# Kernel tuning notes

Measured on AMD Instinct MI355X. Metric: run time of the kernel, lower is better.

The kernel has to match this reference:

```python
import jax, jax.numpy as jnp
from jax import lax
import numpy as np

H = 32  # hidden size
IN = 3  # input dim
NCLASS = 7
T = 30  # sequence length used by forward (indexes t=29)


def _lstm_layer(x, W_ih, W_hh, b_ih, b_hh):
    """One unidirectional LSTM layer, batch_first x: [B,T,D] -> [B,T,H].
    PyTorch gate order: i, f, g, o."""
    B = x.shape[0]
    # Precompute input contribution for all timesteps: [B,T,4H]
    xg = jnp.einsum('btd,gd->btg', x, W_ih) + b_ih + b_hh

    def step(carry, xg_t):
        h, c = carry
        gates = xg_t + h @ W_hh.T  # [B,4H]
        i, f, g, o = jnp.split(gates, 4, axis=-1)
        i = jax.nn.sigmoid(i)
        f = jax.nn.sigmoid(f)
        g = jnp.tanh(g)
        o = jax.nn.sigmoid(o)
        c = f * c + i * g
        h = o * jnp.tanh(c)
        return (h, c), h

    h0 = jnp.zeros((B, H), x.dtype)
    (_, _), hs = lax.scan(step, (h0, h0), jnp.swapaxes(xg, 0, 1))  # hs: [T,B,H]
    return jnp.swapaxes(hs, 0, 1)


def setup_inputs() -> dict:
    key = jax.random.key(0)
    ks = jax.random.split(key, 20)
    B = 65536
    s = 1.0 / np.sqrt(H)  # PyTorch LSTM/Linear init scale
    u = lambda k, shape: jax.random.uniform(k, shape, jnp.float32, -s, s)
    inp = {'X': jax.random.normal(ks[0], (B, T, IN), jnp.float32)}
    dims_in = [IN, H, H]
    for l in range(3):
        inp[f'W_ih{l}'] = u(ks[1 + 4 * l], (4 * H, dims_in[l]))
        inp[f'W_hh{l}'] = u(ks[2 + 4 * l], (4 * H, H))
        inp[f'b_ih{l}'] = u(ks[3 + 4 * l], (4 * H,))
        inp[f'b_hh{l}'] = u(ks[4 + 4 * l], (4 * H,))
    inp['W1'] = u(ks[13], (H // 2, H))
    inp['b1'] = u(ks[14], (H // 2,))
    inp['W2'] = u(ks[15], (NCLASS, H // 2))
    inp['b2'] = u(ks[16], (NCLASS,))
    return inp


def reference(X, W_ih0, W_hh0, b_ih0, b_hh0, W_ih1, W_hh1, b_ih1, b_hh1,
              W_ih2, W_hh2, b_ih2, b_hh2, W1, b1, W2, b2):
    h = _lstm_layer(X, W_ih0, W_hh0, b_ih0, b_hh0)
    h = _lstm_layer(h, W_ih1, W_hh1, b_ih1, b_hh1)
    h = _lstm_layer(h, W_ih2, W_hh2, b_ih2, b_hh2)
    last = h[:, T - 1, :]  # [B,H]
    out = last @ W1.T + b1
    out = out @ W2.T + b2  # [B,7]; Softmax is defined but not applied in forward
    return out
```

## Files before the change

kernel.cpp:

```cpp
#include <hip/hip_runtime.h>
#include <stdint.h>

#define T_STEPS 30
#define BTOT 65536
#define L2E 1.4426950408889634f

typedef __bf16 bf16_t;
typedef bf16_t bf16x8 __attribute__((ext_vector_type(8)));
typedef float f32x4 __attribute__((ext_vector_type(4)));

__device__ __forceinline__ float exp2_fast(float x) {
#if __has_builtin(__builtin_amdgcn_exp2f)
    return __builtin_amdgcn_exp2f(x);
#else
    return __expf(x * 0.6931471805599453f);
#endif
}
__device__ __forceinline__ float rcp_fast(float x) {
    return __builtin_amdgcn_rcpf(x);
}

template <int LI, bool SAVE>
__device__ __forceinline__ void cell(
    int lane, int lrow, int kgrp,
    const bf16_t* __restrict__ wb,
    const float (&bs)[3][8],
    bf16x8 ain,
    bf16x8& ah,
    float (&cst)[3][2][4],
    float (&hsave)[2][4],
    bf16_t* __restrict__ hb)
{
    constexpr int WIH_OFF = ((LI == 0) ? 0 : (LI == 1) ? 2 : 4) * 4096;
    constexpr int WHH_OFF = WIH_OFF + 4096;

    f32x4 z;
    z[0] = 0.0f; z[1] = 0.0f; z[2] = 0.0f; z[3] = 0.0f;
    f32x4 acc[8];
#pragma unroll
    for (int tl = 0; tl < 8; ++tl) {
        bf16x8 bfr = *(const bf16x8*)(wb + WIH_OFF + (tl << 9) + (lane << 3));
        acc[tl] = __builtin_amdgcn_mfma_f32_16x16x32_bf16(ain, bfr, z, 0, 0, 0);
    }
#pragma unroll
    for (int tl = 0; tl < 8; ++tl) {
        bf16x8 bfr = *(const bf16x8*)(wb + WHH_OFF + (tl << 9) + (lane << 3));
        acc[tl] = __builtin_amdgcn_mfma_f32_16x16x32_bf16(ah, bfr, acc[tl], 0, 0, 0);
    }
#pragma unroll
    for (int mt = 0; mt < 2; ++mt) {
#pragma unroll
        for (int r = 0; r < 4; ++r) {
            const float Ae = exp2_fast(acc[0 + mt][r] * (-L2E) + bs[LI][0 + mt]);
            const float Fe = exp2_fast(acc[2 + mt][r] * (-L2E) + bs[LI][2 + mt]);
            const float Be = exp2_fast(acc[4 + mt][r] * (-2.0f * L2E) + bs[LI][4 + mt]);
            const float Oe = exp2_fast(acc[6 + mt][r] * (-L2E) + bs[LI][6 + mt]);
            const float pA = 1.0f + Ae, pF = 1.0f + Fe, pB = 1.0f + Be, pO = 1.0f + Oe;
            const float nB = 1.0f - Be;
            const float t1 = pA * pB;
            const float D  = t1 * pF;
            const float N  = __builtin_fmaf(cst[LI][mt][r], t1, nB * pF);
            const float cc = N * rcp_fast(D);
            cst[LI][mt][r] = cc;
            const float Ce = exp2_fast(cc * (-2.0f * L2E));
            const float pC = 1.0f + Ce, nC = 1.0f - Ce;
            const float hv = nC * rcp_fast(pO * pC);
            if (SAVE) hsave[mt][r] = hv;
            hb[(kgrp * 4 + r) * 40 + mt * 16 + lrow] = (bf16_t)hv;
        }
    }
    ah = *(const bf16x8*)(hb + lrow * 40 + (kgrp << 3));
}

__global__ __launch_bounds__(512, 4) void lstm3_fused(
    const float* __restrict__ X,
    const float* __restrict__ Wih0, const float* __restrict__ Whh0,
    const float* __restrict__ bih0, const float* __restrict__ bhh0,
    const float* __restrict__ Wih1, const float* __restrict__ Whh1,
    const float* __restrict__ bih1, const float* __restrict__ bhh1,
    const float* __restrict__ Wih2, const float* __restrict__ Whh2,
    const float* __restrict__ bih2, const float* __restrict__ bhh2,
    const float* __restrict__ W1, const float* __restrict__ b1,
    const float* __restrict__ W2, const float* __restrict__ b2,
    float* __restrict__ out)
{
    __shared__ alignas(16) bf16_t wfrag[6 * 4096];
    __shared__ float bias_s[3][128];
    __shared__ alignas(16) bf16_t hbuf[8][16 * 40];
    __shared__ float hfin[8][16][33];

    const int tid = threadIdx.x;

    auto stage = [&](int mat, const float* __restrict__ w, int K) {
        for (int p = tid; p < 4096; p += 512) {
            const int tile = p >> 9;
            const int r = p & 511;
            const int ln = r >> 3;
            const int j = r & 7;
            const int k = ((ln >> 4) << 3) + j;
            const int n = (tile << 4) + (ln & 15);
            const float v = (k < K) ? w[n * K + k] : 0.0f;
            wfrag[mat * 4096 + p] = (bf16_t)v;
        }
    };
    stage(0, Wih0, 3);
    stage(1, Whh0, 32);
    stage(2, Wih1, 32);
    stage(3, Whh1, 32);
    stage(4, Wih2, 32);
    stage(5, Whh2, 32);
    for (int p = tid; p < 384; p += 512) {
        const int l = p >> 7, n = p & 127;
        float v;
        if (l == 0)      v = bih0[n] + bhh0[n];
        else if (l == 1) v = bih1[n] + bhh1[n];
        else             v = bih2[n] + bhh2[n];
        bias_s[l][n] = v;
    }
    __syncthreads();

    const int wave = tid >> 6;
    const int lane = tid & 63;
    const int lrow = lane & 15;
    const int kgrp = lane >> 4;
    const int b0   = blockIdx.x * 128 + wave * 16;

    float bs[3][8];
#pragma unroll
    for (int l = 0; l < 3; ++l)
#pragma unroll
        for (int tl = 0; tl < 8; ++tl)
            bs[l][tl] = bias_s[l][tl * 16 + lrow] *
                        (((tl >> 1) == 2) ? (-2.0f * L2E) : (-L2E));

    float cst[3][2][4];
    float h2keep[2][4];
#pragma unroll
    for (int l = 0; l < 3; ++l)
#pragma unroll
        for (int mt = 0; mt < 2; ++mt)
#pragma unroll
            for (int r = 0; r < 4; ++r) cst[l][mt][r] = 0.0f;
#pragma unroll
    for (int mt = 0; mt < 2; ++mt)
#pragma unroll
        for (int r = 0; r < 4; ++r) h2keep[mt][r] = 0.0f;

    bf16x8 ah0, ah1, ah2;
#pragma unroll
    for (int j = 0; j < 8; ++j) {
        ah0[j] = (bf16_t)0.0f; ah1[j] = (bf16_t)0.0f; ah2[j] = (bf16_t)0.0f;
    }

    bf16_t* hb = &hbuf[wave][0];

    const float* xlane = X + (size_t)(b0 + lrow) * (T_STEPS * 3);
    float cx0 = xlane[0], cx1 = xlane[1], cx2 = xlane[2];

    for (int t = 0; t < T_STEPS; ++t) {
        const int tn = (t < T_STEPS - 1) ? (t + 1) : (T_STEPS - 1);
        const float nx0 = xlane[tn * 3 + 0];
        const float nx1 = xlane[tn * 3 + 1];
        const float nx2 = xlane[tn * 3 + 2];

        unsigned lz = 0;
        asm volatile("" : "+v"(lz));
        const bf16_t* wbt = wfrag + lz;

        bf16x8 ax;
#pragma unroll
        for (int j = 0; j < 8; ++j) ax[j] = (bf16_t)0.0f;
        if (kgrp == 0) { ax[0] = (bf16_t)cx0; ax[1] = (bf16_t)cx1; ax[2] = (bf16_t)cx2; }

        cell<0, false>(lane, lrow, kgrp, wbt, bs, ax,  ah0, cst, h2keep, hb);
        cell<1, false>(lane, lrow, kgrp, wbt, bs, ah0, ah1, cst, h2keep, hb);
        cell<2, true >(lane, lrow, kgrp, wbt, bs, ah1, ah2, cst, h2keep, hb);

        cx0 = nx0; cx1 = nx1; cx2 = nx2;
    }

#pragma unroll
    for (int mt = 0; mt < 2; ++mt)
#pragma unroll
        for (int r = 0; r < 4; ++r)
            hfin[wave][kgrp * 4 + r][mt * 16 + lrow] = h2keep[mt][r];

    if (lane < 16) {
        float hv[32];
#pragma unroll
        for (int k = 0; k < 32; ++k) hv[k] = hfin[wave][lane][k];
        float y1[16];
#pragma unroll
        for (int o = 0; o < 16; ++o) {
            float a = b1[o];
#pragma unroll
            for (int k = 0; k < 32; ++k) a += hv[k] * W1[o * 32 + k];
            y1[o] = a;
        }
        const int b = b0 + lane;
#pragma unroll
        for (int q = 0; q < 7; ++q) {
            float a = b2[q];
#pragma unroll
            for (int o = 0; o < 16; ++o) a += y1[o] * W2[q * 16 + o];
            out[b * 7 + q] = a;
        }
    }
}

extern "C" void kernel_launch(void* const* d_in, const int* in_sizes, int n_in,
                              void* d_out, int out_size, void* d_ws, size_t ws_size,
                              hipStream_t stream) {
    (void)in_sizes; (void)n_in; (void)d_ws; (void)ws_size; (void)out_size;
    const float* X    = (const float*)d_in[0];
    const float* Wih0 = (const float*)d_in[1];
    const float* Whh0 = (const float*)d_in[2];
    const float* bih0 = (const float*)d_in[3];
    const float* bhh0 = (const float*)d_in[4];
    const float* Wih1 = (const float*)d_in[5];
    const float* Whh1 = (const float*)d_in[6];
    const float* bih1 = (const float*)d_in[7];
    const float* bhh1 = (const float*)d_in[8];
    const float* Wih2 = (const float*)d_in[9];
    const float* Whh2 = (const float*)d_in[10];
    const float* bih2 = (const float*)d_in[11];
    const float* bhh2 = (const float*)d_in[12];
    const float* W1   = (const float*)d_in[13];
    const float* b1   = (const float*)d_in[14];
    const float* W2   = (const float*)d_in[15];
    const float* b2   = (const float*)d_in[16];
    float* out = (float*)d_out;

    dim3 grid(BTOT / 128), block(512);
    hipLaunchKernelGGL(lstm3_fused, grid, block, 0, stream,
                       X, Wih0, Whh0, bih0, bhh0, Wih1, Whh1, bih1, bhh1,
                       Wih2, Whh2, bih2, bhh2, W1, b1, W2, b2, out);
}
```

Before: 294.7 us.

## Replace exp-based gate activations with packed rational tanh approximations

Rewrites the LSTM gate nonlinearities as Padé-style rational tanh approximations, with sigmoid expressed as 0.5*(1+tanh(x/2)). The numerators and denominators are combined algebraically so each cell update needs only two reciprocals. Values are handled as float2 pairs so the compiler can emit packed FMA/mul instructions. This targets the transcendental (exp) instruction cost in the serial recurrence. In exchange it adds more polynomial FMAs and an approximation error that grows for large gate inputs, since only the cell-state tanh input is clamped.

```diff
diff --git a/kernel.cpp b/kernel.cpp
--- a/kernel.cpp
+++ b/kernel.cpp
@@ -3,32 +3,46 @@
 
 #define T_STEPS 30
 #define BTOT 65536
-#define L2E 1.4426950408889634f
 
 typedef __bf16 bf16_t;
 typedef bf16_t bf16x8 __attribute__((ext_vector_type(8)));
 typedef float f32x4 __attribute__((ext_vector_type(4)));
-
-__device__ __forceinline__ float exp2_fast(float x) {
-#if __has_builtin(__builtin_amdgcn_exp2f)
-    return __builtin_amdgcn_exp2f(x);
-#else
-    return __expf(x * 0.6931471805599453f);
-#endif
-}
-__device__ __forceinline__ float rcp_fast(float x) {
-    return __builtin_amdgcn_rcpf(x);
+typedef float f32x2 __attribute__((ext_vector_type(2)));
+
+__device__ __forceinline__ f32x2 pk(float x) { return f32x2{x, x}; }
+__device__ __forceinline__ f32x2 rcp_pk(f32x2 d) {
+    f32x2 r;
+    r[0] = __builtin_amdgcn_rcpf(d[0]);
+    r[1] = __builtin_amdgcn_rcpf(d[1]);
+    return r;
+}
+__device__ __forceinline__ void tanh_pq(f32x2 y, f32x2& P, f32x2& Q) {
+    const f32x2 u = y * y;
+    f32x2 p = u + pk(378.0f);
+    p = __builtin_elementwise_fma(p, u, pk(17325.0f));
+    p = __builtin_elementwise_fma(p, u, pk(135135.0f));
+    P = p * y;
+    f32x2 q = __builtin_elementwise_fma(u, pk(28.0f), pk(3150.0f));
+    q = __builtin_elementwise_fma(q, u, pk(62370.0f));
+    Q = __builtin_elementwise_fma(q, u, pk(135135.0f));
+}
+__device__ __forceinline__ f32x2 clamp_pk(f32x2 y) {
+    f32x2 r;
+    r[0] = __builtin_amdgcn_fmed3f(y[0], -4.75f, 4.75f);
+    r[1] = __builtin_amdgcn_fmed3f(y[1], -4.75f, 4.75f);
+    return r;
 }
 
 template <int LI, bool SAVE>
 __device__ __forceinline__ void cell(
     int lane, int lrow, int kgrp,
     const bf16_t* __restrict__ wb,
-    const float (&bs)[3][8],
+    const f32x2 (&bsig)[3][3],
+    const f32x2 (&bg)[3],
     bf16x8 ain,
     bf16x8& ah,
-    float (&cst)[3][2][4],
-    float (&hsave)[2][4],
+    f32x2 (&cst)[3][4],
+    f32x2 (&hsave)[4],
     bf16_t* __restrict__ hb)
 {
     constexpr int WIH_OFF = ((LI == 0) ? 0 : (LI == 1) ? 2 : 4) * 4096;
@@ -48,26 +62,37 @@
         acc[tl] = __builtin_amdgcn_mfma_f32_16x16x32_bf16(ah, bfr, acc[tl], 0, 0, 0);
     }
 #pragma unroll
-    for (int mt = 0; mt < 2; ++mt) {
-#pragma unroll
-        for (int r = 0; r < 4; ++r) {
-            const float Ae = exp2_fast(acc[0 + mt][r] * (-L2E) + bs[LI][0 + mt]);
-            const float Fe = exp2_fast(acc[2 + mt][r] * (-L2E) + bs[LI][2 + mt]);
-            const float Be = exp2_fast(acc[4 + mt][r] * (-2.0f * L2E) + bs[LI][4 + mt]);
-            const float Oe = exp2_fast(acc[6 + mt][r] * (-L2E) + bs[LI][6 + mt]);
-            const float pA = 1.0f + Ae, pF = 1.0f + Fe, pB = 1.0f + Be, pO = 1.0f + Oe;
-            const float nB = 1.0f - Be;
-            const float t1 = pA * pB;
-            const float D  = t1 * pF;
-            const float N  = __builtin_fmaf(cst[LI][mt][r], t1, nB * pF);
-            const float cc = N * rcp_fast(D);
-            cst[LI][mt][r] = cc;
-            const float Ce = exp2_fast(cc * (-2.0f * L2E));
-            const float pC = 1.0f + Ce, nC = 1.0f - Ce;
-            const float hv = nC * rcp_fast(pO * pC);
-            if (SAVE) hsave[mt][r] = hv;
-            hb[(kgrp * 4 + r) * 40 + mt * 16 + lrow] = (bf16_t)hv;
-        }
+    for (int r = 0; r < 4; ++r) {
+        const f32x2 a_i = {acc[0][r], acc[1][r]};
+        const f32x2 a_f = {acc[2][r], acc[3][r]};
+        const f32x2 a_g = {acc[4][r], acc[5][r]};
+        const f32x2 a_o = {acc[6][r], acc[7][r]};
+        const f32x2 yi = __builtin_elementwise_fma(a_i, pk(0.5f), bsig[LI][0]);
+        const f32x2 yf = __builtin_elementwise_fma(a_f, pk(0.5f), bsig[LI][1]);
+        const f32x2 yg = a_g + bg[LI];
+        const f32x2 yo = __builtin_elementwise_fma(a_o, pk(0.5f), bsig[LI][2]);
+        f32x2 Pi, Qi, Pf, Qf, Pg, Qg, Po, Qo;
+        tanh_pq(yi, Pi, Qi);
+        tanh_pq(yf, Pf, Qf);
+        tanh_pq(yg, Pg, Qg);
+        tanh_pq(yo, Po, Qo);
+        const f32x2 sf  = Qf + Pf;
+        const f32x2 si  = Qi + Pi;
+        const f32x2 qig = Qi * Qg;
+        const f32x2 m1  = sf * cst[LI][r];
+        const f32x2 m2  = (si * Pg) * Qf;
+        const f32x2 N   = __builtin_elementwise_fma(m1, qig, m2);
+        const f32x2 D2  = (qig * Qf) * pk(2.0f);
+        const f32x2 cc  = N * rcp_pk(D2);
+        cst[LI][r] = cc;
+        f32x2 Pc, Qc;
+        tanh_pq(clamp_pk(cc), Pc, Qc);
+        const f32x2 hn  = (Qo + Po) * Pc;
+        const f32x2 hd2 = (Qo * Qc) * pk(2.0f);
+        const f32x2 hv  = hn * rcp_pk(hd2);
+        if (SAVE) hsave[r] = hv;
+        hb[(kgrp * 4 + r) * 40 + lrow]      = (bf16_t)hv[0];
+        hb[(kgrp * 4 + r) * 40 + 16 + lrow] = (bf16_t)hv[1];
     }
     ah = *(const bf16x8*)(hb + lrow * 40 + (kgrp << 3));
 }
@@ -125,26 +150,27 @@
     const int kgrp = lane >> 4;
     const int b0   = blockIdx.x * 128 + wave * 16;
 
-    float bs[3][8];
+    f32x2 bsig[3][3];
+    f32x2 bg[3];
+#pragma unroll
+    for (int l = 0; l < 3; ++l) {
+#pragma unroll
+        for (int g = 0; g < 3; ++g) {
+            const int base = (g == 2) ? 96 : g * 32;
+            bsig[l][g] = f32x2{0.5f * bias_s[l][base + lrow],
+                               0.5f * bias_s[l][base + 16 + lrow]};
+        }
+        bg[l] = f32x2{bias_s[l][64 + lrow], bias_s[l][80 + lrow]};
+    }
+
+    f32x2 cst[3][4];
+    f32x2 h2keep[4];
 #pragma unroll
     for (int l = 0; l < 3; ++l)
 #pragma unroll
-        for (int tl = 0; tl < 8; ++tl)
-            bs[l][tl] = bias_s[l][tl * 16 + lrow] *
-                        (((tl >> 1) == 2) ? (-2.0f * L2E) : (-L2E));
-
-    float cst[3][2][4];
-    float h2keep[2][4];
-#pragma unroll
-    for (int l = 0; l < 3; ++l)
-#pragma unroll
-        for (int mt = 0; mt < 2; ++mt)
-#pragma unroll
-            for (int r = 0; r < 4; ++r) cst[l][mt][r] = 0.0f;
-#pragma unroll
-    for (int mt = 0; mt < 2; ++mt)
-#pragma unroll
-        for (int r = 0; r < 4; ++r) h2keep[mt][r] = 0.0f;
+        for (int r = 0; r < 4; ++r) cst[l][r] = pk(0.0f);
+#pragma unroll
+    for (int r = 0; r < 4; ++r) h2keep[r] = pk(0.0f);
 
     bf16x8 ah0, ah1, ah2;
 #pragma unroll
@@ -172,18 +198,18 @@
         for (int j = 0; j < 8; ++j) ax[j] = (bf16_t)0.0f;
         if (kgrp == 0) { ax[0] = (bf16_t)cx0; ax[1] = (bf16_t)cx1; ax[2] = (bf16_t)cx2; }
 
-        cell<0, false>(lane, lrow, kgrp, wbt, bs, ax,  ah0, cst, h2keep, hb);
-        cell<1, false>(lane, lrow, kgrp, wbt, bs, ah0, ah1, cst, h2keep, hb);
-        cell<2, true >(lane, lrow, kgrp, wbt, bs, ah1, ah2, cst, h2keep, hb);
+        cell<0, false>(lane, lrow, kgrp, wbt, bsig, bg, ax,  ah0, cst, h2keep, hb);
+        cell<1, false>(lane, lrow, kgrp, wbt, bsig, bg, ah0, ah1, cst, h2keep, hb);
+        cell<2, true >(lane, lrow, kgrp, wbt, bsig, bg, ah1, ah2, cst, h2keep, hb);
 
         cx0 = nx0; cx1 = nx1; cx2 = nx2;
     }
 
 #pragma unroll
-    for (int mt = 0; mt < 2; ++mt)
-#pragma unroll
-        for (int r = 0; r < 4; ++r)
-            hfin[wave][kgrp * 4 + r][mt * 16 + lrow] = h2keep[mt][r];
+    for (int r = 0; r < 4; ++r) {
+        hfin[wave][kgrp * 4 + r][lrow]      = h2keep[r][0];
+        hfin[wave][kgrp * 4 + r][16 + lrow] = h2keep[r][1];
+    }
 
     if (lane < 16) {
         float hv[32];
```

Measured after the change: 369.0 us. +25.2%, slower.

## Keep layer-2 Whh in registers, stage h as fp32 with packed bf16 convert

Applied to the files above, without the earlier changes.

Layer 2's recurrent weight fragments are now loaded once into registers instead of being read from LDS every step, which cuts LDS traffic and footprint. The hidden-state exchange buffer becomes fp32 with a stride of 38 and is converted to bf16 with v_cvt_pk_bf16_f32 on readback, so the separate hfin buffer is no longer needed. Waves also get staggered s_sleep starts to desynchronize LDS access. The extra registers held by whh2 could pressure occupancy under the 512x4 launch bounds.

```diff
diff --git a/kernel.cpp b/kernel.cpp
--- a/kernel.cpp
+++ b/kernel.cpp
@@ -8,6 +8,8 @@
 typedef __bf16 bf16_t;
 typedef bf16_t bf16x8 __attribute__((ext_vector_type(8)));
 typedef float f32x4 __attribute__((ext_vector_type(4)));
+typedef float f32x2 __attribute__((ext_vector_type(2)));
+typedef uint32_t u32x4 __attribute__((ext_vector_type(4)));
 
 __device__ __forceinline__ float exp2_fast(float x) {
 #if __has_builtin(__builtin_amdgcn_exp2f)
@@ -20,19 +22,19 @@
     return __builtin_amdgcn_rcpf(x);
 }
 
-template <int LI, bool SAVE>
+template <int LI>
 __device__ __forceinline__ void cell(
     int lane, int lrow, int kgrp,
     const bf16_t* __restrict__ wb,
-    const float (&bs)[3][8],
+    const bf16x8* __restrict__ whh2,
+    const float (&bsL)[8],
     bf16x8 ain,
     bf16x8& ah,
-    float (&cst)[3][2][4],
-    float (&hsave)[2][4],
-    bf16_t* __restrict__ hb)
+    float (&cst)[2][4],
+    float* __restrict__ hb)
 {
     constexpr int WIH_OFF = ((LI == 0) ? 0 : (LI == 1) ? 2 : 4) * 4096;
-    constexpr int WHH_OFF = WIH_OFF + 4096;
+    constexpr int WHH_OFF = ((LI == 0) ? 1 : 3) * 4096;
 
     f32x4 z;
     z[0] = 0.0f; z[1] = 0.0f; z[2] = 0.0f; z[3] = 0.0f;
@@ -44,32 +46,47 @@
     }
 #pragma unroll
     for (int tl = 0; tl < 8; ++tl) {
-        bf16x8 bfr = *(const bf16x8*)(wb + WHH_OFF + (tl << 9) + (lane << 3));
+        bf16x8 bfr;
+        if constexpr (LI == 2) {
+            bfr = whh2[tl];
+        } else {
+            bfr = *(const bf16x8*)(wb + WHH_OFF + (tl << 9) + (lane << 3));
+        }
         acc[tl] = __builtin_amdgcn_mfma_f32_16x16x32_bf16(ah, bfr, acc[tl], 0, 0, 0);
     }
 #pragma unroll
     for (int mt = 0; mt < 2; ++mt) {
 #pragma unroll
         for (int r = 0; r < 4; ++r) {
-            const float Ae = exp2_fast(acc[0 + mt][r] * (-L2E) + bs[LI][0 + mt]);
-            const float Fe = exp2_fast(acc[2 + mt][r] * (-L2E) + bs[LI][2 + mt]);
-            const float Be = exp2_fast(acc[4 + mt][r] * (-2.0f * L2E) + bs[LI][4 + mt]);
-            const float Oe = exp2_fast(acc[6 + mt][r] * (-L2E) + bs[LI][6 + mt]);
+            const float Ae = exp2_fast(acc[0 + mt][r] * (-L2E) + bsL[0 + mt]);
+            const float Fe = exp2_fast(acc[2 + mt][r] * (-L2E) + bsL[2 + mt]);
+            const float Be = exp2_fast(acc[4 + mt][r] * (-2.0f * L2E) + bsL[4 + mt]);
+            const float Oe = exp2_fast(acc[6 + mt][r] * (-L2E) + bsL[6 + mt]);
             const float pA = 1.0f + Ae, pF = 1.0f + Fe, pB = 1.0f + Be, pO = 1.0f + Oe;
             const float nB = 1.0f - Be;
             const float t1 = pA * pB;
             const float D  = t1 * pF;
-            const float N  = __builtin_fmaf(cst[LI][mt][r], t1, nB * pF);
+            const float N  = __builtin_fmaf(cst[mt][r], t1, nB * pF);
             const float cc = N * rcp_fast(D);
-            cst[LI][mt][r] = cc;
+            cst[mt][r] = cc;
             const float Ce = exp2_fast(cc * (-2.0f * L2E));
-            const float pC = 1.0f + Ce, nC = 1.0f - Ce;
-            const float hv = nC * rcp_fast(pO * pC);
-            if (SAVE) hsave[mt][r] = hv;
-            hb[(kgrp * 4 + r) * 40 + mt * 16 + lrow] = (bf16_t)hv;
-        }
-    }
-    ah = *(const bf16x8*)(hb + lrow * 40 + (kgrp << 3));
+            const float hv = (1.0f - Ce) * rcp_fast(pO * (1.0f + Ce));
+            hb[(kgrp * 4 + r) * 38 + mt * 16 + lrow] = hv;
+        }
+    }
+    const float* rb = hb + lrow * 38 + (kgrp << 3);
+    const f32x2 w0 = *(const f32x2*)(rb + 0);
+    const f32x2 w1 = *(const f32x2*)(rb + 2);
+    const f32x2 w2 = *(const f32x2*)(rb + 4);
+    const f32x2 w3 = *(const f32x2*)(rb + 6);
+    uint32_t d0, d1, d2, d3;
+    asm("v_cvt_pk_bf16_f32 %0, %1, %2" : "=v"(d0) : "v"(w0[0]), "v"(w0[1]));
+    asm("v_cvt_pk_bf16_f32 %0, %1, %2" : "=v"(d1) : "v"(w1[0]), "v"(w1[1]));
+    asm("v_cvt_pk_bf16_f32 %0, %1, %2" : "=v"(d2) : "v"(w2[0]), "v"(w2[1]));
+    asm("v_cvt_pk_bf16_f32 %0, %1, %2" : "=v"(d3) : "v"(w3[0]), "v"(w3[1]));
+    u32x4 u;
+    u[0] = d0; u[1] = d1; u[2] = d2; u[3] = d3;
+    ah = __builtin_bit_cast(bf16x8, u);
 }
 
 __global__ __launch_bounds__(512, 4) void lstm3_fused(
@@ -84,10 +101,9 @@
     const float* __restrict__ W2, const float* __restrict__ b2,
     float* __restrict__ out)
 {
-    __shared__ alignas(16) bf16_t wfrag[6 * 4096];
+    __shared__ alignas(16) bf16_t wfrag[5 * 4096];
     __shared__ float bias_s[3][128];
-    __shared__ alignas(16) bf16_t hbuf[8][16 * 40];
-    __shared__ float hfin[8][16][33];
+    __shared__ alignas(16) float hbuf32[8][16 * 38];
 
     const int tid = threadIdx.x;
 
@@ -108,7 +124,6 @@
     stage(2, Wih1, 32);
     stage(3, Whh1, 32);
     stage(4, Wih2, 32);
-    stage(5, Whh2, 32);
     for (int p = tid; p < 384; p += 512) {
         const int l = p >> 7, n = p & 127;
         float v;
@@ -125,6 +140,24 @@
     const int kgrp = lane >> 4;
     const int b0   = blockIdx.x * 128 + wave * 16;
 
+    bf16x8 whh2[8];
+#pragma unroll
+    for (int tl = 0; tl < 8; ++tl) {
+        const int n = tl * 16 + lrow;
+        const float* q = Whh2 + n * 32 + kgrp * 8;
+        bf16x8 f;
+#pragma unroll
+        for (int j = 0; j < 8; ++j) f[j] = (bf16_t)q[j];
+        whh2[tl] = f;
+    }
+
+    switch (wave & 3) {
+        case 1: __builtin_amdgcn_s_sleep(4);  break;
+        case 2: __builtin_amdgcn_s_sleep(8);  break;
+        case 3: __builtin_amdgcn_s_sleep(12); break;
+        default: break;
+    }
+
     float bs[3][8];
 #pragma unroll
     for (int l = 0; l < 3; ++l)
@@ -134,17 +167,12 @@
                         (((tl >> 1) == 2) ? (-2.0f * L2E) : (-L2E));
 
     float cst[3][2][4];
-    float h2keep[2][4];
 #pragma unroll
     for (int l = 0; l < 3; ++l)
 #pragma unroll
         for (int mt = 0; mt < 2; ++mt)
 #pragma unroll
             for (int r = 0; r < 4; ++r) cst[l][mt][r] = 0.0f;
-#pragma unroll
-    for (int mt = 0; mt < 2; ++mt)
-#pragma unroll
-        for (int r = 0; r < 4; ++r) h2keep[mt][r] = 0.0f;
 
     bf16x8 ah0, ah1, ah2;
 #pragma unroll
@@ -152,7 +180,7 @@
         ah0[j] = (bf16_t)0.0f; ah1[j] = (bf16_t)0.0f; ah2[j] = (bf16_t)0.0f;
     }
 
-    bf16_t* hb = &hbuf[wave][0];
+    float* hb = &hbuf32[wave][0];
 
     const float* xlane = X + (size_t)(b0 + lrow) * (T_STEPS * 3);
     float cx0 = xlane[0], cx1 = xlane[1], cx2 = xlane[2];
@@ -172,23 +200,18 @@
         for (int j = 0; j < 8; ++j) ax[j] = (bf16_t)0.0f;
         if (kgrp == 0) { ax[0] = (bf16_t)cx0; ax[1] = (bf16_t)cx1; ax[2] = (bf16_t)cx2; }
 
-        cell<0, false>(lane, lrow, kgrp, wbt, bs, ax,  ah0, cst, h2keep, hb);
-        cell<1, false>(lane, lrow, kgrp, wbt, bs, ah0, ah1, cst, h2keep, hb);
-        cell<2, true >(lane, lrow, kgrp, wbt, bs, ah1, ah2, cst, h2keep, hb);
+        cell<0>(lane, lrow, kgrp, wbt, whh2, bs[0], ax,  ah0, cst[0], hb);
+        cell<1>(lane, lrow, kgrp, wbt, whh2, bs[1], ah0, ah1, cst[1], hb);
+        cell<2>(lane, lrow, kgrp, wbt, whh2, bs[2], ah1, ah2, cst[2], hb);
 
         cx0 = nx0; cx1 = nx1; cx2 = nx2;
     }
 
-#pragma unroll
-    for (int mt = 0; mt < 2; ++mt)
-#pragma unroll
-        for (int r = 0; r < 4; ++r)
-            hfin[wave][kgrp * 4 + r][mt * 16 + lrow] = h2keep[mt][r];
-
     if (lane < 16) {
+        const float* hrow = hb + lane * 38;
         float hv[32];
 #pragma unroll
-        for (int k = 0; k < 32; ++k) hv[k] = hfin[wave][lane][k];
+        for (int k = 0; k < 32; ++k) hv[k] = hrow[k];
         float y1[16];
 #pragma unroll
         for (int o = 0; o < 16; ++o) {
```

Result: slower. 319.2 us (+8.3%).

## Split each LSTM cell's gate tiles across wave pairs with shared h exchange

Applied to the files above, without the earlier changes.

Each batch tile of 16 rows is now handled by a pair of waves, each computing half the hidden units (4 of 8 gate tiles), exchanging h through double-buffered shared memory with a block barrier after every cell. This halves per-wave MFMA and transcendental work on the serial recurrence chain and doubles the number of blocks. Layer-0 input weights use a compact 3-wide fragment instead of a full padded matrix, and occupancy hint rises to 6 blocks. The cost is 90 __syncthreads per sequence and half as many batch rows per block.

```diff
diff --git a/kernel.cpp b/kernel.cpp
--- a/kernel.cpp
+++ b/kernel.cpp
@@ -8,6 +8,8 @@
 typedef __bf16 bf16_t;
 typedef bf16_t bf16x8 __attribute__((ext_vector_type(8)));
 typedef float f32x4 __attribute__((ext_vector_type(4)));
+typedef uint32_t u32x2 __attribute__((ext_vector_type(2)));
+typedef uint32_t u32x4 __attribute__((ext_vector_type(4)));
 
 __device__ __forceinline__ float exp2_fast(float x) {
 #if __has_builtin(__builtin_amdgcn_exp2f)
@@ -20,59 +22,66 @@
     return __builtin_amdgcn_rcpf(x);
 }
 
-template <int LI, bool SAVE>
-__device__ __forceinline__ void cell(
-    int lane, int lrow, int kgrp,
+template <int MIH, int MHH, bool X0>
+__device__ __forceinline__ void cellS(
+    int lane, int lrow, int kgrp, int q,
     const bf16_t* __restrict__ wb,
-    const float (&bs)[3][8],
+    const bf16_t* __restrict__ w0,
+    const float (&bsL)[4],
     bf16x8 ain,
     bf16x8& ah,
-    float (&cst)[3][2][4],
-    float (&hsave)[2][4],
-    bf16_t* __restrict__ hb)
+    float (&cst)[4],
+    float (&h2k)[4], bool sv,
+    bf16_t* __restrict__ hbw)
 {
-    constexpr int WIH_OFF = ((LI == 0) ? 0 : (LI == 1) ? 2 : 4) * 4096;
-    constexpr int WHH_OFF = WIH_OFF + 4096;
-
     f32x4 z;
     z[0] = 0.0f; z[1] = 0.0f; z[2] = 0.0f; z[3] = 0.0f;
-    f32x4 acc[8];
-#pragma unroll
-    for (int tl = 0; tl < 8; ++tl) {
-        bf16x8 bfr = *(const bf16x8*)(wb + WIH_OFF + (tl << 9) + (lane << 3));
-        acc[tl] = __builtin_amdgcn_mfma_f32_16x16x32_bf16(ain, bfr, z, 0, 0, 0);
-    }
-#pragma unroll
-    for (int tl = 0; tl < 8; ++tl) {
-        bf16x8 bfr = *(const bf16x8*)(wb + WHH_OFF + (tl << 9) + (lane << 3));
-        acc[tl] = __builtin_amdgcn_mfma_f32_16x16x32_bf16(ah, bfr, acc[tl], 0, 0, 0);
-    }
-#pragma unroll
-    for (int mt = 0; mt < 2; ++mt) {
-#pragma unroll
-        for (int r = 0; r < 4; ++r) {
-            const float Ae = exp2_fast(acc[0 + mt][r] * (-L2E) + bs[LI][0 + mt]);
-            const float Fe = exp2_fast(acc[2 + mt][r] * (-L2E) + bs[LI][2 + mt]);
-            const float Be = exp2_fast(acc[4 + mt][r] * (-2.0f * L2E) + bs[LI][4 + mt]);
-            const float Oe = exp2_fast(acc[6 + mt][r] * (-L2E) + bs[LI][6 + mt]);
-            const float pA = 1.0f + Ae, pF = 1.0f + Fe, pB = 1.0f + Be, pO = 1.0f + Oe;
-            const float nB = 1.0f - Be;
-            const float t1 = pA * pB;
-            const float D  = t1 * pF;
-            const float N  = __builtin_fmaf(cst[LI][mt][r], t1, nB * pF);
-            const float cc = N * rcp_fast(D);
-            cst[LI][mt][r] = cc;
-            const float Ce = exp2_fast(cc * (-2.0f * L2E));
-            const float pC = 1.0f + Ce, nC = 1.0f - Ce;
-            const float hv = nC * rcp_fast(pO * pC);
-            if (SAVE) hsave[mt][r] = hv;
-            hb[(kgrp * 4 + r) * 40 + mt * 16 + lrow] = (bf16_t)hv;
-        }
-    }
-    ah = *(const bf16x8*)(hb + lrow * 40 + (kgrp << 3));
-}
-
-__global__ __launch_bounds__(512, 4) void lstm3_fused(
+    f32x4 acc[4];
+#pragma unroll
+    for (int G = 0; G < 4; ++G) {
+        const int tile = 2 * G + q;
+        bf16x8 fi;
+        if constexpr (X0) {
+            u32x2 u;
+            u[0] = 0u; u[1] = 0u;
+            if (kgrp == 0) u = *(const u32x2*)(w0 + (tile * 16 + lrow) * 4);
+            u32x4 uu;
+            uu[0] = u[0]; uu[1] = u[1]; uu[2] = 0u; uu[3] = 0u;
+            fi = __builtin_bit_cast(bf16x8, uu);
+        } else {
+            fi = *(const bf16x8*)(wb + MIH * 4096 + (tile << 9) + (lane << 3));
+        }
+        acc[G] = __builtin_amdgcn_mfma_f32_16x16x32_bf16(ain, fi, z, 0, 0, 0);
+    }
+#pragma unroll
+    for (int G = 0; G < 4; ++G) {
+        const int tile = 2 * G + q;
+        bf16x8 fh = *(const bf16x8*)(wb + MHH * 4096 + (tile << 9) + (lane << 3));
+        acc[G] = __builtin_amdgcn_mfma_f32_16x16x32_bf16(ah, fh, acc[G], 0, 0, 0);
+    }
+#pragma unroll
+    for (int r = 0; r < 4; ++r) {
+        const float Ae = exp2_fast(acc[0][r] * (-L2E) + bsL[0]);
+        const float Fe = exp2_fast(acc[1][r] * (-L2E) + bsL[1]);
+        const float Be = exp2_fast(acc[2][r] * (-2.0f * L2E) + bsL[2]);
+        const float Oe = exp2_fast(acc[3][r] * (-L2E) + bsL[3]);
+        const float pA = 1.0f + Ae, pF = 1.0f + Fe, pB = 1.0f + Be, pO = 1.0f + Oe;
+        const float nB = 1.0f - Be;
+        const float t1 = pA * pB;
+        const float D  = t1 * pF;
+        const float N  = __builtin_fmaf(cst[r], t1, nB * pF);
+        const float cc = N * rcp_fast(D);
+        cst[r] = cc;
+        const float Ce = exp2_fast(cc * (-2.0f * L2E));
+        const float hv = (1.0f - Ce) * rcp_fast(pO * (1.0f + Ce));
+        if (sv) h2k[r] = hv;
+        hbw[(kgrp * 4 + r) * 40 + 16 * q + lrow] = (bf16_t)hv;
+    }
+    __syncthreads();
+    ah = *(const bf16x8*)(hbw + lrow * 40 + (kgrp << 3));
+}
+
+__global__ __launch_bounds__(512, 6) void lstm3_split(
     const float* __restrict__ X,
     const float* __restrict__ Wih0, const float* __restrict__ Whh0,
     const float* __restrict__ bih0, const float* __restrict__ bhh0,
@@ -84,14 +93,13 @@
     const float* __restrict__ W2, const float* __restrict__ b2,
     float* __restrict__ out)
 {
-    __shared__ alignas(16) bf16_t wfrag[6 * 4096];
-    __shared__ float bias_s[3][128];
-    __shared__ alignas(16) bf16_t hbuf[8][16 * 40];
-    __shared__ float hfin[8][16][33];
+    __shared__ alignas(16) bf16_t wfrag[5 * 4096];
+    __shared__ alignas(8)  bf16_t w0c[512];
+    __shared__ alignas(16) bf16_t hxch[4][2][16 * 40];
 
     const int tid = threadIdx.x;
 
-    auto stage = [&](int mat, const float* __restrict__ w, int K) {
+    auto stage = [&](int mat, const float* __restrict__ w) {
         for (int p = tid; p < 4096; p += 512) {
             const int tile = p >> 9;
             const int r = p & 511;
@@ -99,52 +107,51 @@
             const int j = r & 7;
             const int k = ((ln >> 4) << 3) + j;
             const int n = (tile << 4) + (ln & 15);
-            const float v = (k < K) ? w[n * K + k] : 0.0f;
-            wfrag[mat * 4096 + p] = (bf16_t)v;
+            wfrag[mat * 4096 + p] = (bf16_t)w[n * 32 + k];
         }
     };
-    stage(0, Wih0, 3);
-    stage(1, Whh0, 32);
-    stage(2, Wih1, 32);
-    stage(3, Whh1, 32);
-    stage(4, Wih2, 32);
-    stage(5, Whh2, 32);
-    for (int p = tid; p < 384; p += 512) {
-        const int l = p >> 7, n = p & 127;
-        float v;
-        if (l == 0)      v = bih0[n] + bhh0[n];
-        else if (l == 1) v = bih1[n] + bhh1[n];
-        else             v = bih2[n] + bhh2[n];
-        bias_s[l][n] = v;
+    stage(0, Whh0);
+    stage(1, Wih1);
+    stage(2, Whh1);
+    stage(3, Wih2);
+    stage(4, Whh2);
+    {
+        const int p = tid;
+        if (p < 512) {
+            const int t8 = p >> 6;
+            const int lr = (p >> 2) & 15;
+            const int k  = p & 3;
+            w0c[p] = (k < 3) ? (bf16_t)Wih0[(t8 * 16 + lr) * 3 + k] : (bf16_t)(0.0f);
+        }
     }
     __syncthreads();
 
     const int wave = tid >> 6;
     const int lane = tid & 63;
+    const int pair = wave >> 1;
+    const int q    = wave & 1;
     const int lrow = lane & 15;
     const int kgrp = lane >> 4;
-    const int b0   = blockIdx.x * 128 + wave * 16;
-
-    float bs[3][8];
+    const int b0   = blockIdx.x * 64 + pair * 16;
+
+    float bs[3][4];
+#pragma unroll
+    for (int G = 0; G < 4; ++G) {
+        const int n = 32 * G + 16 * q + lrow;
+        const float s = (G == 2) ? (-2.0f * L2E) : (-L2E);
+        bs[0][G] = (bih0[n] + bhh0[n]) * s;
+        bs[1][G] = (bih1[n] + bhh1[n]) * s;
+        bs[2][G] = (bih2[n] + bhh2[n]) * s;
+    }
+
+    float cst[3][4];
+    float h2k[4];
 #pragma unroll
     for (int l = 0; l < 3; ++l)
 #pragma unroll
-        for (int tl = 0; tl < 8; ++tl)
-            bs[l][tl] = bias_s[l][tl * 16 + lrow] *
-                        (((tl >> 1) == 2) ? (-2.0f * L2E) : (-L2E));
-
-    float cst[3][2][4];
-    float h2keep[2][4];
-#pragma unroll
-    for (int l = 0; l < 3; ++l)
-#pragma unroll
-        for (int mt = 0; mt < 2; ++mt)
-#pragma unroll
-            for (int r = 0; r < 4; ++r) cst[l][mt][r] = 0.0f;
-#pragma unroll
-    for (int mt = 0; mt < 2; ++mt)
-#pragma unroll
-        for (int r = 0; r < 4; ++r) h2keep[mt][r] = 0.0f;
+        for (int r = 0; r < 4; ++r) cst[l][r] = 0.0f;
+#pragma unroll
+    for (int r = 0; r < 4; ++r) h2k[r] = 0.0f;
 
     bf16x8 ah0, ah1, ah2;
 #pragma unroll
@@ -152,11 +159,10 @@
         ah0[j] = (bf16_t)0.0f; ah1[j] = (bf16_t)0.0f; ah2[j] = (bf16_t)0.0f;
     }
 
-    bf16_t* hb = &hbuf[wave][0];
-
     const float* xlane = X + (size_t)(b0 + lrow) * (T_STEPS * 3);
     float cx0 = xlane[0], cx1 = xlane[1], cx2 = xlane[2];
 
+    int buf = 0;
     for (int t = 0; t < T_STEPS; ++t) {
         const int tn = (t < T_STEPS - 1) ? (t + 1) : (T_STEPS - 1);
         const float nx0 = xlane[tn * 3 + 0];
@@ -166,29 +172,38 @@
         unsigned lz = 0;
         asm volatile("" : "+v"(lz));
         const bf16_t* wbt = wfrag + lz;
+        const bf16_t* w0t = w0c + lz;
 
         bf16x8 ax;
 #pragma unroll
         for (int j = 0; j < 8; ++j) ax[j] = (bf16_t)0.0f;
         if (kgrp == 0) { ax[0] = (bf16_t)cx0; ax[1] = (bf16_t)cx1; ax[2] = (bf16_t)cx2; }
 
-        cell<0, false>(lane, lrow, kgrp, wbt, bs, ax,  ah0, cst, h2keep, hb);
-        cell<1, false>(lane, lrow, kgrp, wbt, bs, ah0, ah1, cst, h2keep, hb);
-        cell<2, true >(lane, lrow, kgrp, wbt, bs, ah1, ah2, cst, h2keep, hb);
+        const bool sv = (t == T_STEPS - 1);
+        cellS<0, 0, true >(lane, lrow, kgrp, q, wbt, w0t, bs[0], ax,  ah0,
+                           cst[0], h2k, false, &hxch[pair][buf][0]);
+        buf ^= 1;
+        cellS<1, 2, false>(lane, lrow, kgrp, q, wbt, w0t, bs[1], ah0, ah1,
+                           cst[1], h2k, false, &hxch[pair][buf][0]);
+        buf ^= 1;
+        cellS<3, 4, false>(lane, lrow, kgrp, q, wbt, w0t, bs[2], ah1, ah2,
+                           cst[2], h2k, sv,    &hxch[pair][buf][0]);
+        buf ^= 1;
 
         cx0 = nx0; cx1 = nx1; cx2 = nx2;
     }
 
-#pragma unroll
-    for (int mt = 0; mt < 2; ++mt)
-#pragma unroll
-        for (int r = 0; r < 4; ++r)
-            hfin[wave][kgrp * 4 + r][mt * 16 + lrow] = h2keep[mt][r];
-
-    if (lane < 16) {
+    float* hf = (float*)wfrag;
+    const int hfo = pair * 528;
+#pragma unroll
+    for (int r = 0; r < 4; ++r)
+        hf[hfo + (kgrp * 4 + r) * 33 + 16 * q + lrow] = h2k[r];
+    __syncthreads();
+
+    if (q == 0 && lane < 16) {
         float hv[32];
 #pragma unroll
-        for (int k = 0; k < 32; ++k) hv[k] = hfin[wave][lane][k];
+        for (int k = 0; k < 32; ++k) hv[k] = hf[hfo + lane * 33 + k];
         float y1[16];
 #pragma unroll
         for (int o = 0; o < 16; ++o) {
@@ -199,11 +214,11 @@
         }
         const int b = b0 + lane;
 #pragma unroll
-        for (int q = 0; q < 7; ++q) {
-            float a = b2[q];
-#pragma unroll
-            for (int o = 0; o < 16; ++o) a += y1[o] * W2[q * 16 + o];
-            out[b * 7 + q] = a;
+        for (int oc = 0; oc < 7; ++oc) {
+            float a = b2[oc];
+#pragma unroll
+            for (int o = 0; o < 16; ++o) a += y1[o] * W2[oc * 16 + o];
+            out[b * 7 + oc] = a;
         }
     }
 }
@@ -231,8 +246,8 @@
     const float* b2   = (const float*)d_in[16];
     float* out = (float*)d_out;
 
-    dim3 grid(BTOT / 128), block(512);
-    hipLaunchKernelGGL(lstm3_fused, grid, block, 0, stream,
+    dim3 grid(BTOT / 64), block(512);
+    hipLaunchKernelGGL(lstm3_split, grid, block, 0, stream,
                        X, Wih0, Whh0, bih0, bhh0, Wih1, Whh1, bih1, bhh1,
                        Wih2, Whh2, bih2, bhh2, W1, b1, W2, b2, out);
 }
```

Result: slower. 312.6 us (+6.1%).
